# Kernel tuning notes

Measured on AMD Instinct MI355X. Metric: run time of the kernel, lower is better.

## Reference

```python
import jax, jax.numpy as jnp
import numpy as np

K = 3        # kernel_size
PAD = 1      # padding ('same' for stride 1)
RANK = 53    # CP rank from compression=10: round(27*32*64/(10*(9+32+64)))


def _kaiming_uniform(key, shape, fan_in):
    # matches nn.init.kaiming_uniform_(a=sqrt(5)): bound = 1/sqrt(fan_in)
    bound = 1.0 / np.sqrt(fan_in)
    return jax.random.uniform(key, shape, jnp.float32, -bound, bound)


def setup_inputs() -> dict:
    key = jax.random.key(0)
    ks = jax.random.split(key, 7)
    B, Cin, Cout, H, W, D = 1, 32, 64, 56, 56, 56
    x = jax.random.normal(ks[0], (B, Cin, H, W, D), jnp.float32)
    # CP factor matrices (fan_in = second dim for torch's 2D kaiming)
    U_kh = _kaiming_uniform(ks[1], (K, RANK), RANK)
    U_kw = _kaiming_uniform(ks[2], (K, RANK), RANK)
    U_kd = _kaiming_uniform(ks[3], (K, RANK), RANK)
    U_cin = _kaiming_uniform(ks[4], (Cin, RANK), RANK)
    U_cout = _kaiming_uniform(ks[5], (RANK, Cout), Cout)
    bias = jax.random.normal(ks[6], (Cout,), jnp.float32)
    return {"x": x, "U_kh": U_kh, "U_kw": U_kw, "U_kd": U_kd,
            "U_cin": U_cin, "U_cout": U_cout, "bias": bias}


def reference(x, U_kh, U_kw, U_kd, U_cin, U_cout, bias):
    B, C, H, W, D = x.shape
    xp = jnp.pad(x, ((0, 0), (0, 0), (PAD, PAD), (PAD, PAD), (PAD, PAD)))
    # im2col patches: patches[i,j,l,b,c,x,y,z] = xp[b,c,x+i,y+j,z+l]
    # (same values/ordering as torch unfold(2).unfold(3).unfold(4), stride=1)
    patches = jnp.stack([
        xp[:, :, i:i + H, j:j + W, l:l + D]
        for i in range(K) for j in range(K) for l in range(K)
    ]).reshape(K, K, K, B, C, H, W, D)
    # CP tensor-network contraction (legs: k_h,k_w,k_d,c_in share rank r -> c_out)
    out = jnp.einsum('ijlbcxyz,ir,jr,lr,cr,ro->boxyz',
                     patches, U_kh, U_kw, U_kd, U_cin, U_cout,
                     optimize=True)
    return out + bias[None, :, None, None, None]
```

## Files before the change

kernel.cpp:

```cpp
#include <hip/hip_runtime.h>


#define NP 175616
#define NP2 87808
#define HSTR 3136
#define H2 1568
#define W2 28
#define CIN 32
#define RK 53
#define RC0 27
#define COUT 64
#define SCR 53

__global__ __launch_bounds__(256) void k0_t(const float* __restrict__ Ucin,
                                            float* __restrict__ Ut)
{
    int t = blockIdx.x * 256 + threadIdx.x;
    if (t < RK * CIN) {
        int r = t >> 5, c = t & 31;
        Ut[t] = Ucin[c * RK + r];
    }
}

__global__ __launch_bounds__(256, 8) void k1d(
    const float* __restrict__ x, const float* __restrict__ Ut,
    const float* __restrict__ Ukd, float* __restrict__ T1d)
{
    const int lane = threadIdx.x & 63;
    const int row  = blockIdx.x * 4 + (threadIdx.x >> 6);
    const int p    = row * 56 + lane;
    const bool act = (lane < 56);
    const int pc   = act ? p : (p - 8);

    float xv[CIN];
#pragma unroll
    for (int c = 0; c < CIN; ++c) xv[c] = x[c * NP + pc];
#pragma unroll
    for (int c = 0; c < CIN; ++c) asm volatile("" : "+v"(xv[c]));

    const int r0 = blockIdx.y * 13;
    const int r1 = (blockIdx.y == 3) ? RK : (r0 + 13);

#pragma unroll 1
    for (int rs = r0; rs < r1; rs += 5) {
        const int nb = (r1 - rs < 5) ? (r1 - rs) : 5;
        float acc[5], lm[5], rp[5];
#pragma unroll
        for (int j = 0; j < 5; ++j) {
            if (j < nb) {
                const float* U = Ut + (rs + j) * CIN;
                float a0 = 0.f, a1 = 0.f, a2 = 0.f, a3 = 0.f;
#pragma unroll
                for (int c = 0; c < CIN; c += 4) {
                    a0 += xv[c]     * U[c];
                    a1 += xv[c + 1] * U[c + 1];
                    a2 += xv[c + 2] * U[c + 2];
                    a3 += xv[c + 3] * U[c + 3];
                }
                acc[j] = (a0 + a1) + (a2 + a3);
            }
        }
#pragma unroll
        for (int j = 0; j < 5; ++j) {
            if (j < nb) {
                lm[j] = __shfl_up(acc[j], 1, 64);
                rp[j] = __shfl_down(acc[j], 1, 64);
            }
        }
#pragma unroll
        for (int j = 0; j < 5; ++j) {
            if (j < nb) {
                const int r = rs + j;
                float l  = (lane == 0)  ? 0.f : lm[j];
                float rv = (lane == 55) ? 0.f : rp[j];
                float res = l * Ukd[r] + acc[j] * Ukd[RK + r] + rv * Ukd[2 * RK + r];
                if (act) T1d[(size_t)r * NP + p] = res;
            }
        }
    }
}

__global__ __launch_bounds__(256, 8) void k3z(
    const float2* __restrict__ Ta, const float* __restrict__ Ucout,
    const float* __restrict__ bias, const float* __restrict__ Ukh,
    const float* __restrict__ Ukw, float2* __restrict__ Out)
{
    __shared__ float2 tld[RC0][64];

    const int lane = threadIdx.x & 63;
    const int wv   = threadIdx.x >> 6;

    const int nwg = gridDim.x;
    const int qx = nwg >> 3, rx = nwg & 7;
    const int xcd = blockIdx.x & 7, loc = blockIdx.x >> 3;
    const int swz = ((xcd < rx) ? xcd * (qx + 1) : rx * (qx + 1) + (xcd - rx) * qx) + loc;

    const int bx = swz >> 1;
    const int z  = swz & 1;

    const int q  = bx * 64 + lane;
    const int h  = q / H2;
    const int rm = q - h * H2;
    const int w  = rm / W2;
    const int om = (h > 0)  ? -H2 : 0;
    const int op = (h < 55) ?  H2 : 0;
    const int oa = (w > 0)  ? -W2 : 0;
    const int oc = (w < 55) ?  W2 : 0;
    const float mh0 = (h > 0)  ? 1.f : 0.f;
    const float mh2 = (h < 55) ? 1.f : 0.f;
    const float mw0 = (w > 0)  ? 1.f : 0.f;
    const float mw2 = (w < 55) ? 1.f : 0.f;

    const float2* Sq = Ta + q;
    const int og = __builtin_amdgcn_readfirstlane(z * 32 + (wv << 3));

    float2 a[8];

#pragma unroll 1
    for (int r = wv; r < RC0; r += 4) {
        const float2* S = Sq + (size_t)r * NP2;
        const float kw0 = mw0 * Ukw[r];
        const float kw1 = Ukw[RK + r];
        const float kw2 = mw2 * Ukw[2 * RK + r];
        const float kh0 = mh0 * Ukh[r];
        const float kh1 = Ukh[RK + r];
        const float kh2 = mh2 * Ukh[2 * RK + r];
        float2 v00 = S[om + oa], v01 = S[om], v02 = S[om + oc];
        float2 v10 = S[oa],      v11 = S[0],  v12 = S[oc];
        float2 v20 = S[op + oa], v21 = S[op], v22 = S[op + oc];
        float2 t;
        t.x = (v00.x * kw0 + v01.x * kw1 + v02.x * kw2) * kh0
            + (v10.x * kw0 + v11.x * kw1 + v12.x * kw2) * kh1
            + (v20.x * kw0 + v21.x * kw1 + v22.x * kw2) * kh2;
        t.y = (v00.y * kw0 + v01.y * kw1 + v02.y * kw2) * kh0
            + (v10.y * kw0 + v11.y * kw1 + v12.y * kw2) * kh1
            + (v20.y * kw0 + v21.y * kw1 + v22.y * kw2) * kh2;
        tld[r][lane] = t;
    }
    __syncthreads();

#pragma unroll
    for (int o = 0; o < 8; ++o) {
        float b = bias[og + o];
        a[o].x = b; a[o].y = b;
    }
#pragma unroll 4
    for (int r = 0; r < RC0; ++r) {
        float2 t = tld[r][lane];
        const float* Ur = Ucout + r * COUT + og;
#pragma unroll
        for (int o = 0; o < 8; ++o) {
            float u = Ur[o];
            a[o].x += t.x * u; a[o].y += t.y * u;
        }
    }
    __syncthreads();

#pragma unroll 1
    for (int r = RC0 + wv; r < RK; r += 4) {
        const float2* S = Sq + (size_t)r * NP2;
        const float kw0 = mw0 * Ukw[r];
        const float kw1 = Ukw[RK + r];
        const float kw2 = mw2 * Ukw[2 * RK + r];
        const float kh0 = mh0 * Ukh[r];
        const float kh1 = Ukh[RK + r];
        const float kh2 = mh2 * Ukh[2 * RK + r];
        float2 v00 = S[om + oa], v01 = S[om], v02 = S[om + oc];
        float2 v10 = S[oa],      v11 = S[0],  v12 = S[oc];
        float2 v20 = S[op + oa], v21 = S[op], v22 = S[op + oc];
        float2 t;
        t.x = (v00.x * kw0 + v01.x * kw1 + v02.x * kw2) * kh0
            + (v10.x * kw0 + v11.x * kw1 + v12.x * kw2) * kh1
            + (v20.x * kw0 + v21.x * kw1 + v22.x * kw2) * kh2;
        t.y = (v00.y * kw0 + v01.y * kw1 + v02.y * kw2) * kh0
            + (v10.y * kw0 + v11.y * kw1 + v12.y * kw2) * kh1
            + (v20.y * kw0 + v21.y * kw1 + v22.y * kw2) * kh2;
        tld[r - RC0][lane] = t;
    }
    __syncthreads();

#pragma unroll 4
    for (int r = RC0; r < RK; ++r) {
        float2 t = tld[r - RC0][lane];
        const float* Ur = Ucout + r * COUT + og;
#pragma unroll
        for (int o = 0; o < 8; ++o) {
            float u = Ur[o];
            a[o].x += t.x * u; a[o].y += t.y * u;
        }
    }

#pragma unroll
    for (int o = 0; o < 8; ++o)
        Out[(size_t)(og + o) * NP2 + q] = a[o];
}


__global__ __launch_bounds__(256) void k1_chunk(
    const float* __restrict__ x, const float* __restrict__ Ucin,
    float* T, int r0, int nr)
{
    __shared__ float sU[11 * CIN];
    const int tid = threadIdx.x;
    for (int t = tid; t < nr * CIN; t += 256) {
        int lr = t >> 5, c = t & 31;
        sU[t] = Ucin[c * RK + (r0 + lr)];
    }
    __syncthreads();
    const int p = blockIdx.x * 256 + tid;
    float xv[CIN];
#pragma unroll
    for (int c = 0; c < CIN; ++c) xv[c] = x[c * NP + p];
#pragma unroll 1
    for (int lr = 0; lr < nr; ++lr) {
        float acc = 0.f;
#pragma unroll
        for (int c = 0; c < CIN; ++c) acc += xv[c] * sU[lr * CIN + c];
        T[(size_t)(SCR + lr) * NP + p] = acc;
    }
}

__global__ __launch_bounds__(256) void k2_chunk(
    const float* __restrict__ Ukh, const float* __restrict__ Ukw,
    const float* __restrict__ Ukd, float* T, int r0)
{
    __shared__ float sIn[5800];
    __shared__ float sA[5600];
    const int lr = blockIdx.z;
    const int r  = r0 + lr;
    const int h0 = blockIdx.x * 8, w0 = blockIdx.y * 8;
    const int tid = threadIdx.x;
    const float kh0 = Ukh[r], kh1 = Ukh[RK + r], kh2 = Ukh[2 * RK + r];
    const float kw0 = Ukw[r], kw1 = Ukw[RK + r], kw2 = Ukw[2 * RK + r];
    const float kd0 = Ukd[r], kd1 = Ukd[RK + r], kd2 = Ukd[2 * RK + r];
    const float* T1r = T + (size_t)(SCR + lr) * NP;

    for (int idx = tid; idx < 5800; idx += 256) {
        int d = idx % 58; int t2 = idx / 58; int ww = t2 % 10; int hh = t2 / 10;
        int gh = h0 + hh - 1, gw = w0 + ww - 1, gd = d - 1;
        float v = 0.f;
        if ((unsigned)gh < 56u && (unsigned)gw < 56u && (unsigned)gd < 56u)
            v = T1r[gh * HSTR + gw * 56 + gd];
        sIn[idx] = v;
    }
    __syncthreads();
    for (int idx = tid; idx < 5600; idx += 256) {
        int d = idx % 56; int t2 = idx / 56; int ww = t2 % 10; int hh = t2 / 10;
        const float* b = &sIn[(hh * 10 + ww) * 58 + d];
        sA[idx] = b[0] * kd0 + b[1] * kd1 + b[2] * kd2;
    }
    __syncthreads();
    const float k00 = kh0 * kw0, k01 = kh0 * kw1, k02 = kh0 * kw2;
    const float k10 = kh1 * kw0, k11 = kh1 * kw1, k12 = kh1 * kw2;
    const float k20 = kh2 * kw0, k21 = kh2 * kw1, k22 = kh2 * kw2;
    for (int idx = tid; idx < 3584; idx += 256) {
        int d = idx % 56; int t2 = idx / 56; int ww = t2 % 8; int hh = t2 / 8;
        const float* a = &sA[(hh * 10 + ww) * 56 + d];
        float acc = a[0]    * k00 + a[56]   * k01 + a[112]  * k02
                  + a[560]  * k10 + a[616]  * k11 + a[672]  * k12
                  + a[1120] * k20 + a[1176] * k21 + a[1232] * k22;
        T[(size_t)r * NP + (h0 + hh) * HSTR + (w0 + ww) * 56 + d] = acc;
    }
}

__global__ __launch_bounds__(256) void k3_out(
    float* T, const float* __restrict__ Ucout, const float* __restrict__ bias)
{
    __shared__ float sUo[RK * COUT];
    __shared__ float sB[COUT];
    const int tid = threadIdx.x;
    for (int t = tid; t < RK * COUT; t += 256) sUo[t] = Ucout[t];
    if (tid < COUT) sB[tid] = bias[tid];
    __syncthreads();
    const int p = blockIdx.x * 256 + tid;
    float acc[COUT];
#pragma unroll
    for (int o = 0; o < COUT; ++o) acc[o] = sB[o];
#pragma unroll 1
    for (int r = 0; r < RK; ++r) {
        float t = T[(size_t)r * NP + p];
        const float* Ur = &sUo[r * COUT];
#pragma unroll
        for (int o = 0; o < COUT; ++o) acc[o] += t * Ur[o];
    }
#pragma unroll
    for (int o = 0; o < COUT; ++o) T[(size_t)o * NP + p] = acc[o];
}


extern "C" void kernel_launch(void* const* d_in, const int* in_sizes, int n_in,
                              void* d_out, int out_size, void* d_ws, size_t ws_size,
                              hipStream_t stream)
{
    const float* x     = (const float*)d_in[0];
    const float* Ukh   = (const float*)d_in[1];
    const float* Ukw   = (const float*)d_in[2];
    const float* Ukd   = (const float*)d_in[3];
    const float* Ucin  = (const float*)d_in[4];
    const float* Ucout = (const float*)d_in[5];
    const float* bias  = (const float*)d_in[6];

    const size_t t1_bytes = (size_t)RK * NP * sizeof(float);

    if (ws_size >= t1_bytes + 8192) {
        float* T1 = (float*)d_ws;
        float* Ut = (float*)((char*)d_ws + t1_bytes);
        k0_t<<<7, 256, 0, stream>>>(Ucin, Ut);
        k1d<<<dim3(HSTR / 4, 4), 256, 0, stream>>>(x, Ut, Ukd, T1);
        k3z<<<NP2 / 32, 256, 0, stream>>>((const float2*)T1, Ucout, bias, Ukh,
                                          Ukw, (float2*)d_out);
    } else {
        float* T = (float*)d_out;
        for (int r0 = 0; r0 < RK; r0 += 11) {
            int nr = (RK - r0 < 11) ? (RK - r0) : 11;
            k1_chunk<<<NP / 256, 256, 0, stream>>>(x, Ucin, T, r0, nr);
            k2_chunk<<<dim3(7, 7, nr), 256, 0, stream>>>(Ukh, Ukw, Ukd, T, r0);
        }
        k3_out<<<NP / 256, 256, 0, stream>>>(T, Ucout, bias);
    }
}
```

Before: 174.9 us.

## Merge output-channel halves into one 512-thread block and double-buffer stencil loads

The final stencil+projection kernel now runs 8 waves per block covering all 64 output channels, instead of two blocks each handling 32 channels that both recomputed the same kh/kw stencil over all 53 ranks. This halves the redundant gathers of the intermediate tensor. Each wave also issues the loads for two ranks before blending them, to raise memory-level parallelism. The cost is more registers per thread and a lower occupancy bound (512 threads, 4 blocks per CU).

```diff
diff --git a/kernel.cpp b/kernel.cpp
--- a/kernel.cpp
+++ b/kernel.cpp
@@ -80,7 +80,7 @@
     }
 }
 
-__global__ __launch_bounds__(256, 8) void k3z(
+__global__ __launch_bounds__(512, 4) void k3c2(
     const float2* __restrict__ Ta, const float* __restrict__ Ucout,
     const float* __restrict__ bias, const float* __restrict__ Ukh,
     const float* __restrict__ Ukw, float2* __restrict__ Out)
@@ -95,10 +95,7 @@
     const int xcd = blockIdx.x & 7, loc = blockIdx.x >> 3;
     const int swz = ((xcd < rx) ? xcd * (qx + 1) : rx * (qx + 1) + (xcd - rx) * qx) + loc;
 
-    const int bx = swz >> 1;
-    const int z  = swz & 1;
-
-    const int q  = bx * 64 + lane;
+    const int q  = swz * 64 + lane;
     const int h  = q / H2;
     const int rm = q - h * H2;
     const int w  = rm / W2;
@@ -112,30 +109,39 @@
     const float mw2 = (w < 55) ? 1.f : 0.f;
 
     const float2* Sq = Ta + q;
-    const int og = __builtin_amdgcn_readfirstlane(z * 32 + (wv << 3));
+    const int og = __builtin_amdgcn_readfirstlane(wv << 3);
 
     float2 a[8];
 
-#pragma unroll 1
-    for (int r = wv; r < RC0; r += 4) {
-        const float2* S = Sq + (size_t)r * NP2;
-        const float kw0 = mw0 * Ukw[r];
-        const float kw1 = Ukw[RK + r];
-        const float kw2 = mw2 * Ukw[2 * RK + r];
-        const float kh0 = mh0 * Ukh[r];
-        const float kh1 = Ukh[RK + r];
-        const float kh2 = mh2 * Ukh[2 * RK + r];
-        float2 v00 = S[om + oa], v01 = S[om], v02 = S[om + oc];
-        float2 v10 = S[oa],      v11 = S[0],  v12 = S[oc];
-        float2 v20 = S[op + oa], v21 = S[op], v22 = S[op + oc];
-        float2 t;
-        t.x = (v00.x * kw0 + v01.x * kw1 + v02.x * kw2) * kh0
-            + (v10.x * kw0 + v11.x * kw1 + v12.x * kw2) * kh1
-            + (v20.x * kw0 + v21.x * kw1 + v22.x * kw2) * kh2;
-        t.y = (v00.y * kw0 + v01.y * kw1 + v02.y * kw2) * kh0
-            + (v10.y * kw0 + v11.y * kw1 + v12.y * kw2) * kh1
-            + (v20.y * kw0 + v21.y * kw1 + v22.y * kw2) * kh2;
-        tld[r][lane] = t;
+#define LOAD9(dst, S) { \
+    dst[0] = (S)[om + oa]; dst[1] = (S)[om]; dst[2] = (S)[om + oc]; \
+    dst[3] = (S)[oa];      dst[4] = (S)[0];  dst[5] = (S)[oc];      \
+    dst[6] = (S)[op + oa]; dst[7] = (S)[op]; dst[8] = (S)[op + oc]; }
+
+#define BLEND(dst, t, r) { \
+    const float kw0 = mw0 * Ukw[r]; \
+    const float kw1 = Ukw[RK + (r)]; \
+    const float kw2 = mw2 * Ukw[2 * RK + (r)]; \
+    const float kh0 = mh0 * Ukh[r]; \
+    const float kh1 = Ukh[RK + (r)]; \
+    const float kh2 = mh2 * Ukh[2 * RK + (r)]; \
+    t.x = (dst[0].x * kw0 + dst[1].x * kw1 + dst[2].x * kw2) * kh0 \
+        + (dst[3].x * kw0 + dst[4].x * kw1 + dst[5].x * kw2) * kh1 \
+        + (dst[6].x * kw0 + dst[7].x * kw1 + dst[8].x * kw2) * kh2; \
+    t.y = (dst[0].y * kw0 + dst[1].y * kw1 + dst[2].y * kw2) * kh0 \
+        + (dst[3].y * kw0 + dst[4].y * kw1 + dst[5].y * kw2) * kh1 \
+        + (dst[6].y * kw0 + dst[7].y * kw1 + dst[8].y * kw2) * kh2; }
+
+    float2 vA[9], vB[9];
+
+#pragma unroll 1
+    for (int rb = wv; rb < RC0; rb += 16) {
+        const int rA = rb, rB = rb + 8;
+        const bool hB = (rB < RC0);
+        LOAD9(vA, Sq + (size_t)rA * NP2);
+        if (hB) { LOAD9(vB, Sq + (size_t)rB * NP2); }
+        float2 tA; BLEND(vA, tA, rA); tld[rA][lane] = tA;
+        if (hB) { float2 tB; BLEND(vB, tB, rB); tld[rB][lane] = tB; }
     }
     __syncthreads();
 
@@ -157,25 +163,13 @@
     __syncthreads();
 
 #pragma unroll 1
-    for (int r = RC0 + wv; r < RK; r += 4) {
-        const float2* S = Sq + (size_t)r * NP2;
-        const float kw0 = mw0 * Ukw[r];
-        const float kw1 = Ukw[RK + r];
-        const float kw2 = mw2 * Ukw[2 * RK + r];
-        const float kh0 = mh0 * Ukh[r];
-        const float kh1 = Ukh[RK + r];
-        const float kh2 = mh2 * Ukh[2 * RK + r];
-        float2 v00 = S[om + oa], v01 = S[om], v02 = S[om + oc];
-        float2 v10 = S[oa],      v11 = S[0],  v12 = S[oc];
-        float2 v20 = S[op + oa], v21 = S[op], v22 = S[op + oc];
-        float2 t;
-        t.x = (v00.x * kw0 + v01.x * kw1 + v02.x * kw2) * kh0
-            + (v10.x * kw0 + v11.x * kw1 + v12.x * kw2) * kh1
-            + (v20.x * kw0 + v21.x * kw1 + v22.x * kw2) * kh2;
-        t.y = (v00.y * kw0 + v01.y * kw1 + v02.y * kw2) * kh0
-            + (v10.y * kw0 + v11.y * kw1 + v12.y * kw2) * kh1
-            + (v20.y * kw0 + v21.y * kw1 + v22.y * kw2) * kh2;
-        tld[r - RC0][lane] = t;
+    for (int rb = RC0 + wv; rb < RK; rb += 16) {
+        const int rA = rb, rB = rb + 8;
+        const bool hB = (rB < RK);
+        LOAD9(vA, Sq + (size_t)rA * NP2);
+        if (hB) { LOAD9(vB, Sq + (size_t)rB * NP2); }
+        float2 tA; BLEND(vA, tA, rA); tld[rA - RC0][lane] = tA;
+        if (hB) { float2 tB; BLEND(vB, tB, rB); tld[rB - RC0][lane] = tB; }
     }
     __syncthreads();
 
@@ -193,6 +187,8 @@
 #pragma unroll
     for (int o = 0; o < 8; ++o)
         Out[(size_t)(og + o) * NP2 + q] = a[o];
+#undef LOAD9
+#undef BLEND
 }
 
 
@@ -307,8 +303,8 @@
         float* Ut = (float*)((char*)d_ws + t1_bytes);
         k0_t<<<7, 256, 0, stream>>>(Ucin, Ut);
         k1d<<<dim3(HSTR / 4, 4), 256, 0, stream>>>(x, Ut, Ukd, T1);
-        k3z<<<NP2 / 32, 256, 0, stream>>>((const float2*)T1, Ucout, bias, Ukh,
-                                          Ukw, (float2*)d_out);
+        k3c2<<<NP2 / 64, 512, 0, stream>>>((const float2*)T1, Ucout, bias, Ukh,
+                                           Ukw, (float2*)d_out);
     } else {
         float* T = (float*)d_out;
         for (int r0 = 0; r0 < RK; r0 += 11) {
```

Result: faster. 153.4 us (-12.3%).
